# Kernel tuning notes

Measured on AMD Instinct MI355X. Metric: run time of the kernel, lower is better.

The kernel has to match this reference:

```python
import math
import jax, jax.numpy as jnp
import numpy as np

B, L, DM = 2, 1024, 1024
STATE, EXPAND, CONV, DTR = 16, 2, 4, 8
INNER = DM * EXPAND          # 2048
NFFT = L // 2 + 1            # 513


def _silu(v):
    return v * jax.nn.sigmoid(v)


def setup_inputs() -> dict:
    key = jax.random.key(0)
    ks = jax.random.split(key, 12)
    s = lambda k, shape, sc=0.02: (jax.random.normal(k, shape, jnp.float32) * sc)
    # dt_proj bias initialized like the torch module: exp(U(0,1)*(log dt_max - log dt_min) + log dt_min)
    inv_dt = jnp.exp(jax.random.uniform(ks[10], (INNER,), jnp.float32)
                     * (math.log(0.1) - math.log(0.001)) + math.log(0.001))
    return {
        "x": jax.random.normal(ks[0], (B, L, DM), jnp.float32),
        "in_proj_w": s(ks[1], (2 * INNER, DM)),
        "conv_w": s(ks[2], (INNER, 1, CONV), 0.1),      # depthwise conv kernel
        "conv_b": jnp.zeros((INNER,), jnp.float32),
        "A_log": jnp.tile(jnp.log(jnp.arange(1, STATE + 1, dtype=jnp.float32)), (INNER, 1)),
        "D": jnp.ones((INNER,), jnp.float32),
        "x_proj_w": s(ks[3], (DTR + 2 * STATE, INNER)),
        "dt_proj_w": s(ks[4], (INNER, DTR)),
        "dt_proj_b": inv_dt,
        "filter_real": s(ks[5], (INNER, NFFT)),
        "filter_imag": s(ks[6], (INNER, NFFT)),
        "spectral_decay": jnp.ones((INNER,), jnp.float32) * 0.01,
        "fusion_w": s(ks[7], (INNER, 2 * INNER)),
        "fusion_b": jnp.zeros((INNER,), jnp.float32),
        "out_proj_w": s(ks[8], (DM, INNER)),
        "ln_gamma": jnp.ones((DM,), jnp.float32),
        "ln_beta": jnp.zeros((DM,), jnp.float32),
    }


def reference(x, in_proj_w, conv_w, conv_b, A_log, D, x_proj_w, dt_proj_w, dt_proj_b,
              filter_real, filter_imag, spectral_decay, fusion_w, fusion_b,
              out_proj_w, ln_gamma, ln_beta):
    residual = x
    xz = x @ in_proj_w.T                                   # [B,L,2*INNER]
    x_inner, z = xz[..., :INNER], xz[..., INNER:]
    z = _silu(z)

    # ---- SSM path ----
    xc = jnp.swapaxes(x_inner, 1, 2)                       # [B,E,L]
    xc = jax.lax.conv_general_dilated(
        xc, conv_w, (1,), [(CONV - 1, 0)],                 # causal depthwise conv (pad-left == torch pad + truncate)
        dimension_numbers=("NCH", "OIH", "NCH"),
        feature_group_count=INNER) + conv_b[None, :, None]
    x_conv = jnp.swapaxes(_silu(xc), 1, 2)                 # [B,L,E]

    x_dbc = x_conv @ x_proj_w.T                            # [B,L,DTR+2S]
    dt_x = x_dbc[..., :DTR]
    Bm = x_dbc[..., DTR:DTR + STATE]                       # [B,L,S]
    Cm = x_dbc[..., DTR + STATE:]                          # [B,L,S]
    dt = jax.nn.softplus(dt_x @ dt_proj_w.T + dt_proj_b)   # [B,L,E]
    A = -jnp.exp(A_log)                                    # [E,S]
    dA = jnp.exp(dt[..., None] * A)                        # [B,L,E,S]
    dBx = (dt * x_conv)[..., None] * Bm[:, :, None, :]     # [B,L,E,S]

    def step(h, inp):
        dA_t, dBx_t, C_t = inp
        h = dA_t * h + dBx_t                               # [B,E,S]
        return h, jnp.einsum('bes,bs->be', h, C_t)

    h0 = jnp.zeros((B, INNER, STATE), x.dtype)
    _, ys = jax.lax.scan(step, h0,
                         (jnp.swapaxes(dA, 0, 1), jnp.swapaxes(dBx, 0, 1), jnp.swapaxes(Cm, 0, 1)))
    y_ssm = jnp.swapaxes(ys, 0, 1) + x_conv * D            # [B,L,E]

    # ---- Spectral path ----
    xf = jnp.fft.rfft(jnp.swapaxes(x_inner, 1, 2), axis=-1)        # [B,E,NFFT]
    freqs = jnp.linspace(0.0, 1.0, NFFT)
    filt = (filter_real + 1j * filter_imag) * jnp.exp(-spectral_decay[:, None] * freqs[None, :])
    y_spec = jnp.swapaxes(jnp.fft.irfft(xf * filt[None], n=L, axis=-1), 1, 2)  # [B,L,E]

    # ---- Gated fusion ----
    g = jax.nn.sigmoid(jnp.concatenate([y_ssm, y_spec], -1) @ fusion_w.T + fusion_b)
    y = g * y_ssm + (1.0 - g) * y_spec
    y = y * z
    out = y @ out_proj_w.T + residual                      # [B,L,DM]

    mu = out.mean(-1, keepdims=True)
    var = out.var(-1, keepdims=True)
    return (out - mu) / jnp.sqrt(var + 1e-5) * ln_gamma + ln_beta
```

## Files before the change

kernel.cpp:

```cpp
#include <hip/hip_runtime.h>
#include <math.h>

#define B_ 2
#define L_ 1024
#define DM_ 1024
#define STATE_ 16
#define CONV_ 4
#define DTR_ 8
#define INNER_ 2048
#define M_ (B_*L_)
#define MD_ (B_*INNER_)
#define NFFT_ 513
#define NFP_ 1088
#define NCH_ 32
#define CHL_ 32

typedef unsigned short u16;
typedef __attribute__((ext_vector_type(8))) short short8;
typedef __attribute__((ext_vector_type(8))) __bf16 bf16x8;
typedef __attribute__((ext_vector_type(4))) float f32x4;

__device__ __forceinline__ float frcp_(float x) { return __builtin_amdgcn_rcpf(x); }
__device__ __forceinline__ float fexp_(float x) { return __expf(x); }
__device__ __forceinline__ float fsigm_(float x) { return frcp_(1.f + __expf(-x)); }
__device__ __forceinline__ float fsilu_(float x) { return x * frcp_(1.f + __expf(-x)); }
__device__ __forceinline__ float fsoftplus_(float v) {
  return (v > 20.f) ? v : __logf(1.f + __expf(v));
}
__device__ __forceinline__ u16 f2bf(float f) {
  union { float f; unsigned u; } v; v.f = f;
  unsigned r = v.u + 0x7fffu + ((v.u >> 16) & 1u);
  return (u16)(r >> 16);
}
__device__ __forceinline__ float bf2f(u16 h) {
  union { unsigned u; float f; } v; v.u = ((unsigned)h) << 16;
  return v.f;
}
__device__ __forceinline__ void gload16(const void* g, void* l) {
  __builtin_amdgcn_global_load_lds(
      (const __attribute__((address_space(1))) unsigned*)g,
      (__attribute__((address_space(3))) unsigned*)l, 16, 0, 0);
}
__device__ __forceinline__ f32x4 mfma_bf16(short8 a, short8 b, f32x4 c) {
  return __builtin_amdgcn_mfma_f32_16x16x32_bf16(
      __builtin_bit_cast(bf16x8, a), __builtin_bit_cast(bf16x8, b), c, 0, 0, 0);
}

#define CVT2_N0 2097152
#define CVT2_NT 6291456
__global__ __launch_bounds__(256) void cvt2_k(
    const float* __restrict__ s0, const float* __restrict__ s1,
    u16* __restrict__ out)
{
  int i = (blockIdx.x*256 + threadIdx.x) * 4;
  const float* src; int off;
  if (i < CVT2_N0) { src = s0; off = 0; }
  else             { src = s1; off = CVT2_N0; }
  float4 v = *(const float4*)(src + (i - off));
  ushort4 o;
  o.x = f2bf(v.x); o.y = f2bf(v.y); o.z = f2bf(v.z); o.w = f2bf(v.w);
  *(ushort4*)(out + i) = o;
}

__device__ __forceinline__ void cvt16_body(int eb, int nthr, int t,
    const float* __restrict__ src, u16* __restrict__ dst)
{
  int i = (eb*nthr + t)*16;
  #pragma unroll
  for (int q = 0; q < 4; q++) {
    float4 v = *(const float4*)(src + i + q*4);
    ushort4 o;
    o.x = f2bf(v.x); o.y = f2bf(v.y); o.z = f2bf(v.z); o.w = f2bf(v.w);
    *(ushort4*)(dst + i + q*4) = o;
  }
}

__device__ __forceinline__ void conv_xt_body(int idx, const float* __restrict__ xz,
    const float* __restrict__ cw, const float* __restrict__ cb,
    float* __restrict__ xc, u16* __restrict__ xt)
{
  int c = idx & (INNER_-1);
  int g = idx >> 11;
  int b = g >> 7;
  int lb = (g & 127) * 8;
  float w0=cw[c*4+0], w1=cw[c*4+1], w2=cw[c*4+2], w3=cw[c*4+3];
  float bias = cb[c];
  float v[11];
  #pragma unroll
  for (int j = 0; j < 11; j++) {
    int l = lb - 3 + j;
    v[j] = (l >= 0) ? xz[((size_t)((b << 10) + l))*4096 + c] : 0.f;
  }
  union { u16 a[8]; short8 v8; } tu;
  #pragma unroll
  for (int j = 0; j < 8; j++) tu.a[j] = f2bf(v[j+3]);
  *(short8*)&xt[(((size_t)(b*INNER_ + c)) << 10) + lb] = tu.v8;
  #pragma unroll
  for (int j = 0; j < 8; j++) {
    float s = bias + w0*v[j] + w1*v[j+1] + w2*v[j+2] + w3*v[j+3];
    xc[((size_t)((b << 10) + lb + j))*INNER_ + c] = fsilu_(s);
  }
}

__device__ __forceinline__ void genWdft_body(int idx, u16* __restrict__ W)
{
  int l = idx & (L_-1);
  int col = idx >> 10;
  float v = 0.f;
  int f = col >> 1;
  if (f < NFFT_) {
    int ph = (l*f) & (L_-1);
    float th = (float)ph * (6.283185307179586f / (float)L_);
    v = (col & 1) ? -__sinf(th) : __cosf(th);
  }
  W[idx] = f2bf(v);
}

__device__ __forceinline__ void genWinv_body(int idx, u16* __restrict__ W)
{
  int r = idx % NFP_;
  int l = idx / NFP_;
  int f = r >> 1;
  float v = 0.f;
  if (f < NFFT_) {
    bool edge = (f == 0) || (f == 512);
    float sc = (edge ? 1.f : 2.f) / (float)L_;
    int ph = (f*l) & (L_-1);
    float th = (float)ph * (6.283185307179586f / (float)L_);
    if (r & 1) v = edge ? 0.f : -sc*__sinf(th);
    else       v = sc*__cosf(th);
  }
  W[idx] = f2bf(v);
}

__global__ __launch_bounds__(256) void aux2_k(
    const float* __restrict__ xz, const float* __restrict__ cw,
    const float* __restrict__ cb, float* __restrict__ xc,
    u16* __restrict__ xt, u16* __restrict__ Winv,
    const float* __restrict__ ows, u16* __restrict__ owd,
    const float* __restrict__ xpws, u16* __restrict__ xpwd)
{
  int eb = blockIdx.x;
  if (eb < 2048)      conv_xt_body(eb*256 + threadIdx.x, xz, cw, cb, xc, xt);
  else if (eb < 6400) genWinv_body((eb - 2048)*256 + threadIdx.x, Winv);
  else if (eb < 6912) cvt16_body(eb - 6400, 256, threadIdx.x, ows, owd);
  else                cvt16_body(eb - 6912, 256, threadIdx.x, xpws, xpwd);
}

template<int TM, int TN, int EPI, int YCH, int AUX, int KS>
__global__ __launch_bounds__((TM/64)*(TN/32)*64) void mgemm_k(
    const u16* __restrict__ Ab, const u16* __restrict__ Bb,
    void* __restrict__ Cout, int K, int ldc,
    const float* __restrict__ aux0, u16* __restrict__ aux1,
    const float* __restrict__ aux2, const float* __restrict__ aux3,
    int gx, int gy,
    u16* __restrict__ gw,
    int ldk, const float* __restrict__ cvs, u16* __restrict__ cvd,
    const u16* __restrict__ xga, const u16* __restrict__ xgb,
    float* __restrict__ xgc)
{
  constexpr int WN   = TN/32;
  constexpr int NW   = (TM/64)*WN;
  constexpr int NTHR = NW*64;
  __shared__ __align__(16) u16 As[2][TM*64];
  __shared__ __align__(16) u16 Bs[2][TN*64];
  const int t = threadIdx.x;
  const int nwg = gx * gy;

  bool xg = false;
  int xgi = 0;
  if constexpr (AUX != 0) {
    int eb = (int)blockIdx.x - nwg*KS;
    if (eb >= 0) {
      if constexpr (AUX == 1) {
        if (eb < 2176) genWdft_body(eb*NTHR + t, gw);
        else           cvt16_body(eb - 2176, NTHR, t, cvs, cvd);
        return;
      } else if constexpr (AUX == 3) {
        cvt16_body(eb, NTHR, t, cvs, cvd);
        return;
      } else {
        xg = true; xgi = eb;
      }
    }
  }

  const int lane = t & 63;
  const int w = t >> 6;
  const int wm = w / WN, wn = w % WN;

  const u16* Aop = Ab;
  const u16* Bop = Bb;
  int Kr = K, ldkr = ldk, k0 = 0;
  int M0, N0;
  if (xg) {
    Aop = xga; Bop = xgb; Kr = 2048; ldkr = 2048;
    M0 = xgi * TM; N0 = 0;
  } else {
    int bid = blockIdx.x;
    int ks = 0;
    if constexpr (KS > 1) { ks = bid / nwg; bid -= ks*nwg; }
    k0 = ks * K;
    const int lid = (bid & 7) * (nwg >> 3) + (bid >> 3);
    int bx, by;
    if (YCH) { by = lid / gx; bx = lid - by*gx; }
    else     { bx = lid / gy; by = lid - bx*gy; }
    M0 = by * TM; N0 = bx * TN;
    if constexpr (EPI == 7) {
      Cout = (void*)((float*)Cout + (size_t)ks * ((size_t)gy*TM*ldc));
    } else if constexpr (EPI == 8) {
      Cout = (void*)((u16*)Cout + (size_t)ks * ((size_t)gy*TM*ldc));
    }
  }

  f32x4 acc[4][2] = {};

  auto stage = [&](int buf, int kk0) {
    #pragma unroll
    for (int q = 0; q < TM*8/NTHR; q++) {
      int u = q*NTHR + t;
      int row = u >> 3, gpr = u & 7;
      int grp = gpr ^ (row & 7);
      gload16(Aop + (size_t)(M0+row)*ldkr + k0 + kk0 + grp*8, &As[buf][u*8]);
    }
    #pragma unroll
    for (int q = 0; q < TN*8/NTHR; q++) {
      int u = q*NTHR + t;
      int row = u >> 3, gpr = u & 7;
      int grp = gpr ^ (row & 7);
      gload16(Bop + (size_t)(N0+row)*ldkr + k0 + kk0 + grp*8, &Bs[buf][u*8]);
    }
  };

  stage(0, 0);
  const int nk = Kr >> 6;
  for (int kst = 0; kst < nk; kst++) {
    const int buf = kst & 1;
    __syncthreads();
    if (kst + 1 < nk) stage(buf ^ 1, (kst + 1) << 6);
    const u16* Asb = As[buf];
    const u16* Bsb = Bs[buf];
    #pragma unroll
    for (int kk = 0; kk < 2; kk++) {
      const int quad = lane >> 4;
      const int grp = kk*4 + quad;
      short8 af[4], bfr[2];
      #pragma unroll
      for (int i = 0; i < 4; i++) {
        int row = wm*64 + i*16 + (lane & 15);
        af[i] = *(const short8*)&Asb[(row*8 + (grp ^ (row & 7)))*8];
      }
      #pragma unroll
      for (int j = 0; j < 2; j++) {
        int row = wn*32 + j*16 + (lane & 15);
        bfr[j] = *(const short8*)&Bsb[(row*8 + (grp ^ (row & 7)))*8];
      }
      #pragma unroll
      for (int i = 0; i < 4; i++)
        #pragma unroll
        for (int j = 0; j < 2; j++)
          acc[i][j] = mfma_bf16(af[i], bfr[j], acc[i][j]);
    }
  }

  if (xg) {
    #pragma unroll
    for (int i = 0; i < 4; i++) {
      int mbase = M0 + wm*64 + i*16 + (lane >> 4)*4;
      #pragma unroll
      for (int j = 0; j < 2; j++) {
        int n = wn*32 + j*16 + (lane & 15);
        if (n < 40) {
          #pragma unroll
          for (int r = 0; r < 4; r++)
            xgc[(size_t)(mbase + r)*40 + n] = acc[i][j][r];
        }
      }
    }
    return;
  }

  if constexpr (EPI == 6) {
    u16* T = (u16*)&As[0][0];
    __syncthreads();
    #pragma unroll
    for (int i = 0; i < 4; i++) {
      int cb = wm*64 + i*16 + (lane >> 4)*4;
      #pragma unroll
      for (int j = 0; j < 2; j++) {
        int ll = wn*32 + j*16 + (lane & 15);
        #pragma unroll
        for (int r = 0; r < 4; r++)
          T[(cb + r)*66 + ll] = f2bf(acc[i][j][r]);
      }
    }
    __syncthreads();
    const int b2 = M0 >> 11, c0 = M0 & (INNER_-1);
    u16* yc = (u16*)Cout;
    #pragma unroll
    for (int q = 0; q < (TM*TN/8)/NTHR; q++) {
      int task = q*NTHR + t;
      int cg = task & 15, ll = task >> 4;
      union { u16 a[8]; short8 v8; } tu;
      #pragma unroll
      for (int e = 0; e < 8; e++) tu.a[e] = T[(cg*8 + e)*66 + ll];
      *(short8*)&yc[((size_t)((b2 << 10) + N0 + ll) << 12) + 2048 + c0 + cg*8] = tu.v8;
    }
  } else {
    #pragma unroll
    for (int i = 0; i < 4; i++) {
      int mbase = M0 + wm*64 + i*16 + (lane >> 4)*4;
      #pragma unroll
      for (int j = 0; j < 2; j++) {
        int n = N0 + wn*32 + j*16 + (lane & 15);
        #pragma unroll
        for (int r = 0; r < 4; r++) {
          int m = mbase + r;
          float v = acc[i][j][r];
          if (EPI == 0) {
            ((float*)Cout)[(size_t)m*ldc + n] = v;
          } else if (EPI == 3) {
            float pv = __shfl_xor(v, 1, 64);
            int f = n >> 1;
            float outv = 0.f;
            if (f < NFFT_) {
              int c = m & (INNER_-1);
              float d  = fexp_(-aux2[c] * (float)f * (1.f/512.f));
              float wr = aux0[c*NFFT_+f]*d, wi = aux3[c*NFFT_+f]*d;
              float a = (n & 1) ? pv : v;
              float b = (n & 1) ? v : pv;
              outv = (n & 1) ? (a*wi + b*wr) : (a*wr - b*wi);
            }
            ((u16*)Cout)[(size_t)m*ldc + n] = f2bf(outv);
          } else if (EPI == 7) {
            ((float*)Cout)[(size_t)m*ldc + n] = v;
          } else {
            ((u16*)Cout)[(size_t)m*ldc + n] = f2bf(v);
          }
        }
      }
    }
  }
}

__global__ __launch_bounds__(256) void combine_gate_k(
    const u16* __restrict__ P, const float* __restrict__ fus_b,
    const u16* __restrict__ ycat, const float* __restrict__ xz,
    u16* __restrict__ ycomb)
{
  int i4 = (blockIdx.x*256 + threadIdx.x)*4;
  int m = i4 >> 11, n = i4 & 2047;
  ushort4 p0 = *(const ushort4*)(P + i4);
  ushort4 p1 = *(const ushort4*)(P + 4194304 + i4);
  ushort4 ysv = *(const ushort4*)(ycat + (size_t)m*4096 + n);
  ushort4 ypv = *(const ushort4*)(ycat + (size_t)m*4096 + 2048 + n);
  float4 zv = *(const float4*)(xz + (size_t)m*4096 + 2048 + n);
  float4 fb = *(const float4*)(fus_b + n);
  float pp[4] = {bf2f(p0.x)+bf2f(p1.x), bf2f(p0.y)+bf2f(p1.y),
                 bf2f(p0.z)+bf2f(p1.z), bf2f(p0.w)+bf2f(p1.w)};
  float zz[4] = {zv.x, zv.y, zv.z, zv.w};
  float bb[4] = {fb.x, fb.y, fb.z, fb.w};
  u16 ys[4] = {ysv.x, ysv.y, ysv.z, ysv.w};
  u16 yp[4] = {ypv.x, ypv.y, ypv.z, ypv.w};
  ushort4 o;
  u16* op = (u16*)&o;
  #pragma unroll
  for (int j = 0; j < 4; j++) {
    float g = fsigm_(pp[j] + bb[j]);
    op[j] = f2bf((g*bf2f(ys[j]) + (1.f-g)*bf2f(yp[j]))*fsilu_(zz[j]));
  }
  *(ushort4*)(ycomb + i4) = o;
}

__global__ __launch_bounds__(256) void scan1_k(
    const float* __restrict__ xdbc, const float* __restrict__ xconv,
    const float* __restrict__ A_log, const float* __restrict__ dtw,
    const float* __restrict__ dtb, float* __restrict__ Pq)
{
  int idx = blockIdx.x*256 + threadIdx.x;
  int e  = idx & (INNER_-1);
  int bc = idx >> 11;
  int ch = bc & (NCH_-1);
  int b  = bc >> 5;
  float A[STATE_];
  #pragma unroll
  for (int s=0;s<STATE_;s++) A[s] = -fexp_(A_log[e*STATE_+s]);
  float w[DTR_];
  #pragma unroll
  for (int r=0;r<DTR_;r++) w[r] = dtw[e*DTR_+r];
  float bias = dtb[e];
  float h[STATE_] = {};
  float sdt = 0.f;
  int mbase = b*L_ + ch*CHL_;
  float dtx[DTR_], Bv[STATE_], xcv;
  {
    const float* row = xdbc + (size_t)mbase*40;
    #pragma unroll
    for (int r=0;r<DTR_;r++) dtx[r] = row[r];
    #pragma unroll
    for (int s=0;s<STATE_;s++) Bv[s] = row[8+s];
    xcv = xconv[(size_t)mbase*INNER_ + e];
  }
  for (int l=0;l<CHL_;l++) {
    float ndtx[DTR_], nBv[STATE_], nxcv = 0.f;
    if (l+1 < CHL_) {
      const float* nrow = xdbc + (size_t)(mbase+l+1)*40;
      #pragma unroll
      for (int r=0;r<DTR_;r++) ndtx[r] = nrow[r];
      #pragma unroll
      for (int s=0;s<STATE_;s++) nBv[s] = nrow[8+s];
      nxcv = xconv[(size_t)(mbase+l+1)*INNER_ + e];
    } else {
      #pragma unroll
      for (int r=0;r<DTR_;r++) ndtx[r] = 0.f;
      #pragma unroll
      for (int s=0;s<STATE_;s++) nBv[s] = 0.f;
    }
    float v = bias;
    #pragma unroll
    for (int r=0;r<DTR_;r++) v += dtx[r]*w[r];
    float dt = fsoftplus_(v);
    sdt += dt;
    float dx = dt * xcv;
    #pragma unroll
    for (int s=0;s<STATE_;s++) {
      float dA = fexp_(dt*A[s]);
      h[s] = dA*h[s] + dx*Bv[s];
    }
    #pragma unroll
    for (int r=0;r<DTR_;r++) dtx[r] = ndtx[r];
    #pragma unroll
    for (int s=0;s<STATE_;s++) Bv[s] = nBv[s];
    xcv = nxcv;
  }
  float* o = Pq + (size_t)idx*32;
  #pragma unroll
  for (int s=0;s<STATE_;s++) { o[s] = fexp_(A[s]*sdt); o[16+s] = h[s]; }
}

__global__ __launch_bounds__(256) void scan2_k(float* __restrict__ Pq)
{
  int idx = blockIdx.x*256 + threadIdx.x;
  int s = idx & 15;
  int e = (idx >> 4) & (INNER_-1);
  int b = idx >> 15;
  float h = 0.f;
  for (int ch = 0; ch < NCH_; ch++) {
    size_t base = ((size_t)(b*NCH_+ch)*INNER_ + e)*32;
    float p = Pq[base + s];
    float q = Pq[base + 16 + s];
    Pq[base + 16 + s] = h;
    h = p*h + q;
  }
}

__global__ __launch_bounds__(256) void scan3_k(
    const float* __restrict__ xdbc, const float* __restrict__ xconv,
    const float* __restrict__ A_log, const float* __restrict__ dtw,
    const float* __restrict__ dtb, const float* __restrict__ Dp,
    const float* __restrict__ Pq, u16* __restrict__ ycat)
{
  int idx = blockIdx.x*256 + threadIdx.x;
  int e  = idx & (INNER_-1);
  int bc = idx >> 11;
  int ch = bc & (NCH_-1);
  int b  = bc >> 5;
  float A[STATE_];
  #pragma unroll
  for (int s=0;s<STATE_;s++) A[s] = -fexp_(A_log[e*STATE_+s]);
  float w[DTR_];
  #pragma unroll
  for (int r=0;r<DTR_;r++) w[r] = dtw[e*DTR_+r];
  float bias = dtb[e];
  float Dv = Dp[e];
  float h[STATE_];
  const float* hi = Pq + (size_t)idx*32 + 16;
  #pragma unroll
  for (int s=0;s<STATE_;s++) h[s] = hi[s];
  int mbase = b*L_ + ch*CHL_;
  float dtx[DTR_], Bv[STATE_], Cv[STATE_], xcv;
  {
    const float* row = xdbc + (size_t)mbase*40;
    #pragma unroll
    for (int r=0;r<DTR_;r++) dtx[r] = row[r];
    #pragma unroll
    for (int s=0;s<STATE_;s++) { Bv[s] = row[8+s]; Cv[s] = row[24+s]; }
    xcv = xconv[(size_t)mbase*INNER_ + e];
  }
  for (int l=0;l<CHL_;l++) {
    float ndtx[DTR_], nBv[STATE_], nCv[STATE_], nxcv = 0.f;
    if (l+1 < CHL_) {
      const float* nrow = xdbc + (size_t)(mbase+l+1)*40;
      #pragma unroll
      for (int r=0;r<DTR_;r++) ndtx[r] = nrow[r];
      #pragma unroll
      for (int s=0;s<STATE_;s++) { nBv[s] = nrow[8+s]; nCv[s] = nrow[24+s]; }
      nxcv = xconv[(size_t)(mbase+l+1)*INNER_ + e];
    } else {
      #pragma unroll
      for (int r=0;r<DTR_;r++) ndtx[r] = 0.f;
      #pragma unroll
      for (int s=0;s<STATE_;s++) { nBv[s] = 0.f; nCv[s] = 0.f; }
    }
    float v = bias;
    #pragma unroll
    for (int r=0;r<DTR_;r++) v += dtx[r]*w[r];
    float dt = fsoftplus_(v);
    float dx = dt * xcv;
    float y = 0.f;
    #pragma unroll
    for (int s=0;s<STATE_;s++) {
      float dA = fexp_(dt*A[s]);
      h[s] = dA*h[s] + dx*Bv[s];
      y += h[s]*Cv[s];
    }
    ycat[(size_t)(mbase+l)*4096 + e] = f2bf(y + xcv*Dv);
    #pragma unroll
    for (int r=0;r<DTR_;r++) dtx[r] = ndtx[r];
    #pragma unroll
    for (int s=0;s<STATE_;s++) { Bv[s] = nBv[s]; Cv[s] = nCv[s]; }
    xcv = nxcv;
  }
}

__global__ __launch_bounds__(256) void ln2_k(const float* __restrict__ Q,
    const float* __restrict__ xres,
    const float* __restrict__ gma, const float* __restrict__ bta,
    float* __restrict__ out)
{
  int m = blockIdx.x;
  float s=0.f, s2=0.f;
  float v[4];
  #pragma unroll
  for (int j=0;j<4;j++) {
    int n = threadIdx.x + j*256;
    size_t idx = (size_t)m*DM_ + n;
    v[j] = Q[idx] + Q[2097152 + idx] + xres[idx];
    s += v[j]; s2 += v[j]*v[j];
  }
  #pragma unroll
  for (int off=32; off>=1; off>>=1) {
    s  += __shfl_down(s, off);
    s2 += __shfl_down(s2, off);
  }
  __shared__ float rs[4], rs2[4], stats[2];
  int wid = threadIdx.x >> 6;
  if ((threadIdx.x & 63) == 0) { rs[wid]=s; rs2[wid]=s2; }
  __syncthreads();
  if (threadIdx.x == 0) {
    float ts  = rs[0]+rs[1]+rs[2]+rs[3];
    float ts2 = rs2[0]+rs2[1]+rs2[2]+rs2[3];
    float mu  = ts/(float)DM_;
    float var = ts2/(float)DM_ - mu*mu;
    stats[0] = mu; stats[1] = rsqrtf(var + 1e-5f);
  }
  __syncthreads();
  float mu = stats[0], rstd = stats[1];
  #pragma unroll
  for (int j=0;j<4;j++) {
    int n = threadIdx.x + j*256;
    out[(size_t)m*DM_ + n] = (v[j]-mu)*rstd*gma[n] + bta[n];
  }
}

extern "C" void kernel_launch(void* const* d_in, const int* in_sizes, int n_in,
                              void* d_out, int out_size, void* d_ws, size_t ws_size,
                              hipStream_t stream)
{
  const float* x       = (const float*)d_in[0];
  const float* in_w    = (const float*)d_in[1];
  const float* conv_w  = (const float*)d_in[2];
  const float* conv_b  = (const float*)d_in[3];
  const float* A_log   = (const float*)d_in[4];
  const float* Dp      = (const float*)d_in[5];
  const float* xproj_w = (const float*)d_in[6];
  const float* dt_w    = (const float*)d_in[7];
  const float* dt_b    = (const float*)d_in[8];
  const float* f_re    = (const float*)d_in[9];
  const float* f_im    = (const float*)d_in[10];
  const float* s_dec   = (const float*)d_in[11];
  const float* fus_w   = (const float*)d_in[12];
  const float* fus_b   = (const float*)d_in[13];
  const float* out_w   = (const float*)d_in[14];
  const float* ln_g    = (const float*)d_in[15];
  const float* ln_b    = (const float*)d_in[16];
  float* out = (float*)d_out;

  float* ws    = (float*)d_ws;
  float* xz    = ws;
  float* xconv = xz    + 8388608;
  float* xdbc  = xconv + 4194304;
  float* Pq    = xdbc  + 81920;
  u16* ub      = (u16*)(Pq + 4194304);
  u16* xb      = ub;
  u16* inwb    = xb    + 2097152;
  u16* fuswb   = inwb  + 4194304;
  u16* outwb   = fuswb + 8388608;
  u16* xt      = outwb + 2097152;
  u16* Wb      = xt    + 4194304;
  u16* XFb     = Wb    + 1114112;
  u16* ycat    = XFb   + 4456448;
  u16* ycomb   = xt;
  u16* Winv    = xb;
  u16* xpwb    = xb + 1114112;
  u16* xcb     = inwb;
  u16* fpart   = (u16*)xconv;
  float* opart = Pq;

  cvt2_k<<<CVT2_NT/1024, 256, 0, stream>>>(x, in_w, xb);

  mgemm_k<128,128,0,0,1,1><<<512 + 2176 + 1024, 512, 0, stream>>>(
      xb, inwb, xz, 1024, 4096, nullptr, nullptr, nullptr, nullptr, 32, 16,
      Wb, 1024, fus_w, fuswb, nullptr, nullptr, nullptr);
  aux2_k<<<6932, 256, 0, stream>>>(xz, conv_w, conv_b, xconv, xt, Winv,
                                   out_w, outwb, xproj_w, xpwb);
  mgemm_k<128,64,3,1,3,1><<<544 + 1024, 256, 0, stream>>>(
      xt, Wb, XFb, 1024, NFP_, f_re, nullptr, s_dec, f_im, 17, 32,
      nullptr, 1024, xconv, xcb, nullptr, nullptr, nullptr);
  mgemm_k<128,64,6,1,5,1><<<512 + 16, 256, 0, stream>>>(
      XFb, Winv, ycat, NFP_, 0, nullptr, nullptr, nullptr, nullptr, 16, 32,
      nullptr, NFP_, nullptr, nullptr, xcb, xpwb, xdbc);
  scan1_k<<<(B_*NCH_*INNER_)/256, 256, 0, stream>>>(xdbc, xconv, A_log, dt_w, dt_b, Pq);
  scan2_k<<<(B_*INNER_*STATE_)/256, 256, 0, stream>>>(Pq);
  scan3_k<<<(B_*NCH_*INNER_)/256, 256, 0, stream>>>(xdbc, xconv, A_log, dt_w, dt_b, Dp, Pq, ycat);
  mgemm_k<128,128,8,0,0,2><<<2*256, 512, 0, stream>>>(
      ycat, fuswb, fpart, 2048, 2048, nullptr, nullptr, nullptr, nullptr, 16, 16,
      nullptr, 4096, nullptr, nullptr, nullptr, nullptr, nullptr);
  combine_gate_k<<<(2048*2048/4)/256, 256, 0, stream>>>(
      fpart, fus_b, ycat, xz, ycomb);
  mgemm_k<64,64,7,1,0,2><<<2*512, 128, 0, stream>>>(
      ycomb, outwb, opart, 1024, 1024, nullptr, nullptr, nullptr, nullptr, 16, 32,
      nullptr, 2048, nullptr, nullptr, nullptr, nullptr, nullptr);
  ln2_k<<<M_, 256, 0, stream>>>(opart, x, ln_g, ln_b, out);
}
```

Measured before the change: 368.6 us.

## Move DFT-matrix gen and fusion-weight convert off in_proj GEMM; split out_proj K four ways

Generating the forward DFT matrix and converting the fusion weights to bf16 move out of the tail blocks of the in_proj GEMM launch and into the initial convert kernel, so the in_proj GEMM runs only its 512 tiles. The out_proj GEMM changes from a 2-way to a 4-way split-K (K=512 per split) to put more workgroups on the device. Layernorm now sums four partials. Partials move to the xconv buffer, which adds extra partial-sum traffic and relies on that buffer being free by then.

```diff
diff --git a/kernel.cpp b/kernel.cpp
--- a/kernel.cpp
+++ b/kernel.cpp
@@ -46,22 +46,6 @@
       __builtin_bit_cast(bf16x8, a), __builtin_bit_cast(bf16x8, b), c, 0, 0, 0);
 }
 
-#define CVT2_N0 2097152
-#define CVT2_NT 6291456
-__global__ __launch_bounds__(256) void cvt2_k(
-    const float* __restrict__ s0, const float* __restrict__ s1,
-    u16* __restrict__ out)
-{
-  int i = (blockIdx.x*256 + threadIdx.x) * 4;
-  const float* src; int off;
-  if (i < CVT2_N0) { src = s0; off = 0; }
-  else             { src = s1; off = CVT2_N0; }
-  float4 v = *(const float4*)(src + (i - off));
-  ushort4 o;
-  o.x = f2bf(v.x); o.y = f2bf(v.y); o.z = f2bf(v.z); o.w = f2bf(v.w);
-  *(ushort4*)(out + i) = o;
-}
-
 __device__ __forceinline__ void cvt16_body(int eb, int nthr, int t,
     const float* __restrict__ src, u16* __restrict__ dst)
 {
@@ -72,33 +56,6 @@
     ushort4 o;
     o.x = f2bf(v.x); o.y = f2bf(v.y); o.z = f2bf(v.z); o.w = f2bf(v.w);
     *(ushort4*)(dst + i + q*4) = o;
-  }
-}
-
-__device__ __forceinline__ void conv_xt_body(int idx, const float* __restrict__ xz,
-    const float* __restrict__ cw, const float* __restrict__ cb,
-    float* __restrict__ xc, u16* __restrict__ xt)
-{
-  int c = idx & (INNER_-1);
-  int g = idx >> 11;
-  int b = g >> 7;
-  int lb = (g & 127) * 8;
-  float w0=cw[c*4+0], w1=cw[c*4+1], w2=cw[c*4+2], w3=cw[c*4+3];
-  float bias = cb[c];
-  float v[11];
-  #pragma unroll
-  for (int j = 0; j < 11; j++) {
-    int l = lb - 3 + j;
-    v[j] = (l >= 0) ? xz[((size_t)((b << 10) + l))*4096 + c] : 0.f;
-  }
-  union { u16 a[8]; short8 v8; } tu;
-  #pragma unroll
-  for (int j = 0; j < 8; j++) tu.a[j] = f2bf(v[j+3]);
-  *(short8*)&xt[(((size_t)(b*INNER_ + c)) << 10) + lb] = tu.v8;
-  #pragma unroll
-  for (int j = 0; j < 8; j++) {
-    float s = bias + w0*v[j] + w1*v[j+1] + w2*v[j+2] + w3*v[j+3];
-    xc[((size_t)((b << 10) + lb + j))*INNER_ + c] = fsilu_(s);
   }
 }
 
@@ -133,6 +90,56 @@
   W[idx] = f2bf(v);
 }
 
+__device__ __forceinline__ void conv_xt_body(int idx, const float* __restrict__ xz,
+    const float* __restrict__ cw, const float* __restrict__ cb,
+    float* __restrict__ xc, u16* __restrict__ xt)
+{
+  int c = idx & (INNER_-1);
+  int g = idx >> 11;
+  int b = g >> 7;
+  int lb = (g & 127) * 8;
+  float w0=cw[c*4+0], w1=cw[c*4+1], w2=cw[c*4+2], w3=cw[c*4+3];
+  float bias = cb[c];
+  float v[11];
+  #pragma unroll
+  for (int j = 0; j < 11; j++) {
+    int l = lb - 3 + j;
+    v[j] = (l >= 0) ? xz[((size_t)((b << 10) + l))*4096 + c] : 0.f;
+  }
+  union { u16 a[8]; short8 v8; } tu;
+  #pragma unroll
+  for (int j = 0; j < 8; j++) tu.a[j] = f2bf(v[j+3]);
+  *(short8*)&xt[(((size_t)(b*INNER_ + c)) << 10) + lb] = tu.v8;
+  #pragma unroll
+  for (int j = 0; j < 8; j++) {
+    float s = bias + w0*v[j] + w1*v[j+1] + w2*v[j+2] + w3*v[j+3];
+    xc[((size_t)((b << 10) + lb + j))*INNER_ + c] = fsilu_(s);
+  }
+}
+
+#define CVT2_N0 2097152
+__global__ __launch_bounds__(256) void cvt3_k(
+    const float* __restrict__ s0, const float* __restrict__ s1,
+    u16* __restrict__ out, u16* __restrict__ Wd,
+    const float* __restrict__ fws, u16* __restrict__ fwd)
+{
+  int eb = blockIdx.x;
+  if (eb < 6144) {
+    int i = (eb*256 + threadIdx.x) * 4;
+    const float* src; int off;
+    if (i < CVT2_N0) { src = s0; off = 0; }
+    else             { src = s1; off = CVT2_N0; }
+    float4 v = *(const float4*)(src + (i - off));
+    ushort4 o;
+    o.x = f2bf(v.x); o.y = f2bf(v.y); o.z = f2bf(v.z); o.w = f2bf(v.w);
+    *(ushort4*)(out + i) = o;
+  } else if (eb < 10496) {
+    genWdft_body((eb - 6144)*256 + threadIdx.x, Wd);
+  } else {
+    cvt16_body(eb - 10496, 256, threadIdx.x, fws, fwd);
+  }
+}
+
 __global__ __launch_bounds__(256) void aux2_k(
     const float* __restrict__ xz, const float* __restrict__ cw,
     const float* __restrict__ cb, float* __restrict__ xc,
@@ -154,7 +161,6 @@
     const float* __restrict__ aux0, u16* __restrict__ aux1,
     const float* __restrict__ aux2, const float* __restrict__ aux3,
     int gx, int gy,
-    u16* __restrict__ gw,
     int ldk, const float* __restrict__ cvs, u16* __restrict__ cvd,
     const u16* __restrict__ xga, const u16* __restrict__ xgb,
     float* __restrict__ xgc)
@@ -172,11 +178,7 @@
   if constexpr (AUX != 0) {
     int eb = (int)blockIdx.x - nwg*KS;
     if (eb >= 0) {
-      if constexpr (AUX == 1) {
-        if (eb < 2176) genWdft_body(eb*NTHR + t, gw);
-        else           cvt16_body(eb - 2176, NTHR, t, cvs, cvd);
-        return;
-      } else if constexpr (AUX == 3) {
+      if constexpr (AUX == 3) {
         cvt16_body(eb, NTHR, t, cvs, cvd);
         return;
       } else {
@@ -523,7 +525,7 @@
   }
 }
 
-__global__ __launch_bounds__(256) void ln2_k(const float* __restrict__ Q,
+__global__ __launch_bounds__(256) void ln4_k(const float* __restrict__ Q,
     const float* __restrict__ xres,
     const float* __restrict__ gma, const float* __restrict__ bta,
     float* __restrict__ out)
@@ -535,7 +537,8 @@
   for (int j=0;j<4;j++) {
     int n = threadIdx.x + j*256;
     size_t idx = (size_t)m*DM_ + n;
-    v[j] = Q[idx] + Q[2097152 + idx] + xres[idx];
+    v[j] = Q[idx] + Q[2097152 + idx] + Q[2*2097152 + idx] + Q[3*2097152 + idx]
+         + xres[idx];
     s += v[j]; s2 += v[j]*v[j];
   }
   #pragma unroll
@@ -605,31 +608,31 @@
   u16* xpwb    = xb + 1114112;
   u16* xcb     = inwb;
   u16* fpart   = (u16*)xconv;
-  float* opart = Pq;
-
-  cvt2_k<<<CVT2_NT/1024, 256, 0, stream>>>(x, in_w, xb);
-
-  mgemm_k<128,128,0,0,1,1><<<512 + 2176 + 1024, 512, 0, stream>>>(
+  float* opart = xconv;
+
+  cvt3_k<<<12544, 256, 0, stream>>>(x, in_w, xb, Wb, fus_w, fuswb);
+
+  mgemm_k<128,128,0,0,0,1><<<512, 512, 0, stream>>>(
       xb, inwb, xz, 1024, 4096, nullptr, nullptr, nullptr, nullptr, 32, 16,
-      Wb, 1024, fus_w, fuswb, nullptr, nullptr, nullptr);
+      1024, nullptr, nullptr, nullptr, nullptr, nullptr);
   aux2_k<<<6932, 256, 0, stream>>>(xz, conv_w, conv_b, xconv, xt, Winv,
                                    out_w, outwb, xproj_w, xpwb);
   mgemm_k<128,64,3,1,3,1><<<544 + 1024, 256, 0, stream>>>(
       xt, Wb, XFb, 1024, NFP_, f_re, nullptr, s_dec, f_im, 17, 32,
-      nullptr, 1024, xconv, xcb, nullptr, nullptr, nullptr);
+      1024, xconv, xcb, nullptr, nullptr, nullptr);
   mgemm_k<128,64,6,1,5,1><<<512 + 16, 256, 0, stream>>>(
       XFb, Winv, ycat, NFP_, 0, nullptr, nullptr, nullptr, nullptr, 16, 32,
-      nullptr, NFP_, nullptr, nullptr, xcb, xpwb, xdbc);
+      NFP_, nullptr, nullptr, xcb, xpwb, xdbc);
   scan1_k<<<(B_*NCH_*INNER_)/256, 256, 0, stream>>>(xdbc, xconv, A_log, dt_w, dt_b, Pq);
   scan2_k<<<(B_*INNER_*STATE_)/256, 256, 0, stream>>>(Pq);
   scan3_k<<<(B_*NCH_*INNER_)/256, 256, 0, stream>>>(xdbc, xconv, A_log, dt_w, dt_b, Dp, Pq, ycat);
   mgemm_k<128,128,8,0,0,2><<<2*256, 512, 0, stream>>>(
       ycat, fuswb, fpart, 2048, 2048, nullptr, nullptr, nullptr, nullptr, 16, 16,
-      nullptr, 4096, nullptr, nullptr, nullptr, nullptr, nullptr);
+      4096, nullptr, nullptr, nullptr, nullptr, nullptr);
   combine_gate_k<<<(2048*2048/4)/256, 256, 0, stream>>>(
       fpart, fus_b, ycat, xz, ycomb);
-  mgemm_k<64,64,7,1,0,2><<<2*512, 128, 0, stream>>>(
-      ycomb, outwb, opart, 1024, 1024, nullptr, nullptr, nullptr, nullptr, 16, 32,
-      nullptr, 2048, nullptr, nullptr, nullptr, nullptr, nullptr);
-  ln2_k<<<M_, 256, 0, stream>>>(opart, x, ln_g, ln_b, out);
-}
+  mgemm_k<64,64,7,1,0,4><<<4*512, 128, 0, stream>>>(
+      ycomb, outwb, opart, 512, 1024, nullptr, nullptr, nullptr, nullptr, 16, 32,
+      2048, nullptr, nullptr, nullptr, nullptr, nullptr);
+  ln4_k<<<M_, 256, 0, stream>>>(opart, x, ln_g, ln_b, out);
+}
```

Measured after the change: 368.0 us. Within noise of the previous version (-0.1%).
